# Performance work log

Measured on AMD Instinct MI355X. Metric: run time of the kernel, lower is better.

## Reference

```python
import jax, jax.numpy as jnp
import numpy as np

B, C, N, E, F = 8, 4, 2048, 512, 2048
EPS = 1e-5
MASK_SCALE = 5.0


def layer_norm(x, gamma, beta):
    mu = jnp.mean(x, axis=-1, keepdims=True)
    var = jnp.mean(jnp.square(x - mu), axis=-1, keepdims=True)
    return (x - mu) * jax.lax.rsqrt(var + EPS) * gamma + beta


def setup_inputs() -> dict:
    key = jax.random.key(0)
    ks = jax.random.split(key, 8)
    src = jax.random.normal(ks[0], (B, C, N, E), dtype=jnp.float32)
    key_padding_mask = jax.random.uniform(ks[1], (B, N), dtype=jnp.float32)
    # FFN params (torch Linear default init scale ~ U(-1/sqrt(fan_in), +))
    W1 = jax.random.normal(ks[2], (E, F), dtype=jnp.float32) / np.sqrt(E)
    b1 = jnp.zeros((F,), dtype=jnp.float32)
    W2 = jax.random.normal(ks[3], (F, E), dtype=jnp.float32) / np.sqrt(F)
    b2 = jnp.zeros((E,), dtype=jnp.float32)
    g1 = jnp.ones((E,), dtype=jnp.float32)
    be1 = jnp.zeros((E,), dtype=jnp.float32)
    g2 = jnp.ones((E,), dtype=jnp.float32)
    be2 = jnp.zeros((E,), dtype=jnp.float32)
    return {"src": src, "key_padding_mask": key_padding_mask,
            "W1": W1, "b1": b1, "W2": W2, "b2": b2,
            "g1": g1, "be1": be1, "g2": g2, "be2": be2}


def reference(src, key_padding_mask, W1, b1, W2, b2, g1, be1, g2, be2):
    # src: [B, C, N, E]; channels batched into one fused attention call
    scale = 1.0 / jnp.sqrt(jnp.asarray(src.shape[-1], src.dtype))
    scores = jnp.einsum('bcne,bcme->bcnm', src, src) * scale  # [B,C,N,N]
    scores = scores - key_padding_mask[:, None, None, :] * MASK_SCALE
    attn = jax.nn.softmax(scores, axis=-1)
    attn_out = jnp.einsum('bcnm,bcme->bcne', attn, src)
    # residual + norm1 (dropout is identity at eval)
    src2 = layer_norm(src + attn_out, g1, be1)
    # feedforward: Linear -> ReLU -> Linear
    ff = jax.nn.relu(jnp.einsum('bcne,ef->bcnf', src2, W1) + b1)
    ff = jnp.einsum('bcnf,fe->bcne', ff, W2) + b2
    out = layer_norm(src2 + ff, g2, be2)
    return out
```

## Files before the change

### kernel.cpp

```cpp
#include <hip/hip_runtime.h>
#include <stdint.h>

constexpr int CB = 8, CC = 4, CN = 2048, CE = 512, CF = 2048;
constexpr long long TOT = (long long)CB * CC * CN * CE;
constexpr int MCH = 32768;
constexpr float SCALE = 0.04419417382415922f;
constexpr float MASK_SCALE = 5.0f;
constexpr float EPS = 1e-5f;

typedef unsigned short bf16_t;
typedef __attribute__((ext_vector_type(4))) float f32x4;
typedef __attribute__((ext_vector_type(8))) short s16x8;

#define DEV static __device__ __forceinline__

DEV unsigned short f2bf(float f) {
    unsigned u = __float_as_uint(f);
    unsigned r = (u + 0x7fffu + ((u >> 16) & 1u)) >> 16;
    return (unsigned short)r;
}
DEV float bf2f(unsigned short b) {
    return __uint_as_float(((unsigned)b) << 16);
}

typedef const __attribute__((address_space(1))) unsigned int* gptr_t;
typedef __attribute__((address_space(3))) unsigned int* lptr_t;
DEV void async16(const void* g, void* l) {
    __builtin_amdgcn_global_load_lds((gptr_t)g, (lptr_t)l, 16, 0, 0);
}

#define FULL_BAR() do { asm volatile("" ::: "memory"); __builtin_amdgcn_s_barrier(); asm volatile("" ::: "memory"); } while (0)
#define LGKM0() asm volatile("s_waitcnt lgkmcnt(0)" ::: "memory")

DEV float blockSum256(float v, float* sm) {
    #pragma unroll
    for (int o = 32; o; o >>= 1) v += __shfl_xor(v, o);
    int w = threadIdx.x >> 6;
    __syncthreads();
    if ((threadIdx.x & 63) == 0) sm[w] = v;
    __syncthreads();
    return sm[0] + sm[1] + sm[2] + sm[3];
}
DEV float blockMax256(float v, float* sm) {
    #pragma unroll
    for (int o = 32; o; o >>= 1) v = fmaxf(v, __shfl_xor(v, o));
    int w = threadIdx.x >> 6;
    __syncthreads();
    if ((threadIdx.x & 63) == 0) sm[w] = v;
    __syncthreads();
    return fmaxf(fmaxf(sm[0], sm[1]), fmaxf(sm[2], sm[3]));
}

__global__ __launch_bounds__(256) void cvt_f32_bf16_vec(
    const float* __restrict__ in, bf16_t* __restrict__ out, long long n) {
    long long i = ((long long)blockIdx.x * 256 + threadIdx.x) * 4;
    long long stride = (long long)gridDim.x * 1024;
    for (; i < n; i += stride) {
        float4 v = *reinterpret_cast<const float4*>(in + i);
        ushort4 u;
        u.x = f2bf(v.x); u.y = f2bf(v.y); u.z = f2bf(v.z); u.w = f2bf(v.w);
        *reinterpret_cast<ushort4*>(out + i) = u;
    }
}

__global__ __launch_bounds__(256) void transpose_f32_bf16(
    const float* __restrict__ in, bf16_t* __restrict__ out,
    int R, int Cc) {
    __shared__ float tile[32][33];
    int rb = blockIdx.y * 32, cb = blockIdx.x * 32;
    int tx = threadIdx.x & 31, ty = threadIdx.x >> 5;
    #pragma unroll
    for (int i = 0; i < 32; i += 8)
        tile[ty + i][tx] = in[(size_t)(rb + ty + i) * Cc + cb + tx];
    __syncthreads();
    #pragma unroll
    for (int i = 0; i < 32; i += 8)
        out[(size_t)(cb + ty + i) * R + rb + tx] = f2bf(tile[tx][ty + i]);
}

__global__ __launch_bounds__(256) void transpose_bf16(
    const bf16_t* __restrict__ in, bf16_t* __restrict__ out,
    int R, int Cc, long long sIn, long long sOut) {
    __shared__ bf16_t tile[32][36];
    const bf16_t* inz = in + (size_t)blockIdx.z * sIn;
    bf16_t* outz = out + (size_t)blockIdx.z * sOut;
    int rb = blockIdx.y * 32, cb = blockIdx.x * 32;
    int t = threadIdx.x;
    int r = t >> 3, c4 = (t & 7) * 4;
    *(ushort4*)&tile[r][c4] = *(const ushort4*)&inz[(size_t)(rb + r) * Cc + cb + c4];
    __syncthreads();
    int c = t >> 3, r4 = (t & 7) * 4;
    ushort4 w;
    w.x = tile[r4 + 0][c]; w.y = tile[r4 + 1][c];
    w.z = tile[r4 + 2][c]; w.w = tile[r4 + 3][c];
    *(ushort4*)&outz[(size_t)(cb + c) * R + rb + r4] = w;
}

template <int EPI>
__global__ __launch_bounds__(512, 2) void gemm256(
    const bf16_t* __restrict__ A, const bf16_t* __restrict__ B,
    void* __restrict__ Cptr, const float* __restrict__ bias, float alpha,
    int M, int Nc, int K, long long sA, long long sB, long long sC) {
    extern __shared__ bf16_t lds[];
    bf16_t* AsL = lds;
    bf16_t* BsL = lds + 32768;

    int bx, by, bz;
    {
        int gx = gridDim.x, gy = gridDim.y;
        int nwg = gx * gy * gridDim.z;
        int flat = blockIdx.x + gx * (blockIdx.y + gy * blockIdx.z);
        int wg = (nwg & 7) ? flat : ((flat & 7) * (nwg >> 3) + (flat >> 3));
        bx = wg % gx;
        int tmp = wg / gx;
        by = tmp % gy;
        bz = tmp / gy;
    }

    const bf16_t* Az = A + (size_t)bz * sA;
    const bf16_t* Bz = B + (size_t)bz * sB;
    const int t = threadIdx.x;
    const int lane = t & 63, wid = t >> 6;
    const int wr = wid >> 2, wc = wid & 3;
    const int brow = by * 256, bcol = bx * 256;
    const int NT = K >> 6;

    const int r0 = t >> 3, s0 = t & 7;
    const int ce = ((s0 ^ (r0 & 7)) << 3);
    const bf16_t* aP0 = Az + (size_t)(brow + r0) * K + ce;
    const bf16_t* bP0 = Bz + (size_t)(bcol + r0) * K + ce;
    const size_t rK64 = (size_t)64 * K;
    const size_t h128K = (size_t)128 * K;

    #define STAGE_A(kt_, h_) do { \
        bf16_t* d_ = AsL + ((((kt_) & 1) * 2 + (h_)) * 8192); \
        const bf16_t* s_ = aP0 + (size_t)(h_) * h128K + (size_t)(kt_) * 64; \
        async16(s_, d_ + t * 8); \
        async16(s_ + rK64, d_ + 4096 + t * 8); \
    } while (0)
    #define STAGE_B(kt_, h_) do { \
        bf16_t* d_ = BsL + ((((kt_) & 1) * 2 + (h_)) * 8192); \
        const bf16_t* s_ = bP0 + (size_t)(h_) * h128K + (size_t)(kt_) * 64; \
        async16(s_, d_ + t * 8); \
        async16(s_ + rK64, d_ + 4096 + t * 8); \
    } while (0)

    const int q = lane >> 4, rr0 = lane & 15, xmask = rr0 & 7;
    s16x8 af[4][2];
    s16x8 bv[2][2][2];
    f32x4 acc[2][2][4][2] = {};

    #define READ_A(ktp_, qm_) do { \
        const bf16_t* base_ = AsL + (((ktp_) * 2 + (qm_)) * 8192); \
        _Pragma("unroll") for (int m_ = 0; m_ < 4; ++m_) \
        _Pragma("unroll") for (int ks_ = 0; ks_ < 2; ++ks_) \
            af[m_][ks_] = *(const s16x8*)(base_ + (wr * 64 + m_ * 16 + rr0) * 64 + (((ks_ * 4 + q) ^ xmask) << 3)); \
    } while (0)
    #define READ_B(ktp_, qn_) do { \
        const bf16_t* base_ = BsL + (((ktp_) * 2 + (qn_)) * 8192); \
        _Pragma("unroll") for (int n_ = 0; n_ < 2; ++n_) \
        _Pragma("unroll") for (int ks_ = 0; ks_ < 2; ++ks_) \
            bv[qn_][n_][ks_] = *(const s16x8*)(base_ + (wc * 32 + n_ * 16 + rr0) * 64 + (((ks_ * 4 + q) ^ xmask) << 3)); \
    } while (0)
    #define MFMA_Q(qm_, qn_) do { \
        __builtin_amdgcn_s_setprio(1); \
        _Pragma("unroll") for (int m_ = 0; m_ < 4; ++m_) \
        _Pragma("unroll") for (int n_ = 0; n_ < 2; ++n_) \
        _Pragma("unroll") for (int ks_ = 0; ks_ < 2; ++ks_) \
            acc[qm_][qn_][m_][n_] = __builtin_amdgcn_mfma_f32_16x16x32_bf16( \
                af[m_][ks_], bv[qn_][n_][ks_], acc[qm_][qn_][m_][n_], 0, 0, 0); \
        __builtin_amdgcn_s_setprio(0); \
    } while (0)

    STAGE_A(0, 0); STAGE_B(0, 0); STAGE_B(0, 1); STAGE_A(0, 1);
    if (1 < NT) {
        STAGE_A(1, 0); STAGE_B(1, 0);
        asm volatile("s_waitcnt vmcnt(4)" ::: "memory");
    } else {
        asm volatile("s_waitcnt vmcnt(0)" ::: "memory");
    }
    FULL_BAR();

    for (int kt = 0; kt < NT; ++kt) {
        const int ktp = kt & 1;
        READ_A(ktp, 0);
        READ_B(ktp, 0);
        if (kt + 1 < NT) STAGE_B(kt + 1, 1);
        FULL_BAR();
        LGKM0();
        MFMA_Q(0, 0);
        FULL_BAR();

        READ_B(ktp, 1);
        if (kt + 1 < NT) STAGE_A(kt + 1, 1);
        FULL_BAR();
        LGKM0();
        MFMA_Q(0, 1);
        FULL_BAR();

        READ_A(ktp, 1);
        if (kt + 2 < NT) STAGE_A(kt + 2, 0);
        FULL_BAR();
        LGKM0();
        MFMA_Q(1, 0);
        FULL_BAR();

        if (kt + 2 < NT) {
            STAGE_B(kt + 2, 0);
            asm volatile("s_waitcnt vmcnt(4)" ::: "memory");
        } else {
            asm volatile("s_waitcnt vmcnt(0)" ::: "memory");
        }
        FULL_BAR();
        MFMA_Q(1, 1);
        FULL_BAR();
    }

    size_t cz = (size_t)bz * sC;
    #pragma unroll
    for (int qm = 0; qm < 2; ++qm)
    #pragma unroll
    for (int qn = 0; qn < 2; ++qn)
    #pragma unroll
    for (int m = 0; m < 4; ++m)
    #pragma unroll
    for (int n = 0; n < 2; ++n) {
        int col = bcol + qn * 128 + wc * 32 + n * 16 + (lane & 15);
        float bvv = (EPI == 1 || EPI == 2) ? bias[col] : 0.f;
        #pragma unroll
        for (int j = 0; j < 4; ++j) {
            int row = brow + qm * 128 + wr * 64 + m * 16 + q * 4 + j;
            float v = acc[qm][qn][m][n][j] + bvv;
            if constexpr (EPI == 1)
                ((bf16_t*)Cptr)[cz + (size_t)row * Nc + col] = f2bf(fmaxf(v, 0.f));
            else if constexpr (EPI == 3)
                ((bf16_t*)Cptr)[cz + (size_t)row * Nc + col] = f2bf(v * alpha);
            else
                ((float*)Cptr)[cz + (size_t)row * Nc + col] = v;
        }
    }
    #undef STAGE_A
    #undef STAGE_B
    #undef READ_A
    #undef READ_B
    #undef MFMA_Q
}

__global__ __launch_bounds__(256) void softmax_bf16(
    bf16_t* __restrict__ S, const float* __restrict__ mask) {
    __shared__ float sm[4];
    int gr = blockIdx.x;
    int b = gr >> 13;
    bf16_t* row = S + (size_t)gr * CN;
    int tid = threadIdx.x;
    const float* mrow = mask + (size_t)b * CN + tid * 8;
    s16x8 v = *(const s16x8*)(row + tid * 8);
    float4 m0 = *(const float4*)(mrow);
    float4 m1 = *(const float4*)(mrow + 4);
    float x[8];
    x[0] = bf2f((unsigned short)v[0]) - m0.x * MASK_SCALE;
    x[1] = bf2f((unsigned short)v[1]) - m0.y * MASK_SCALE;
    x[2] = bf2f((unsigned short)v[2]) - m0.z * MASK_SCALE;
    x[3] = bf2f((unsigned short)v[3]) - m0.w * MASK_SCALE;
    x[4] = bf2f((unsigned short)v[4]) - m1.x * MASK_SCALE;
    x[5] = bf2f((unsigned short)v[5]) - m1.y * MASK_SCALE;
    x[6] = bf2f((unsigned short)v[6]) - m1.z * MASK_SCALE;
    x[7] = bf2f((unsigned short)v[7]) - m1.w * MASK_SCALE;
    float mx = -3.4e38f;
    #pragma unroll
    for (int i = 0; i < 8; i++) mx = fmaxf(mx, x[i]);
    mx = blockMax256(mx, sm);
    float s = 0.f;
    #pragma unroll
    for (int i = 0; i < 8; i++) { x[i] = __expf(x[i] - mx); s += x[i]; }
    s = blockSum256(s, sm);
    float inv = 1.f / s;
    s16x8 u;
    #pragma unroll
    for (int i = 0; i < 8; i++) u[i] = (short)f2bf(x[i] * inv);
    *(s16x8*)(row + tid * 8) = u;
}

__global__ __launch_bounds__(256) void ln1_kernel(
    const bf16_t* __restrict__ src, const bf16_t* __restrict__ ao,
    const float* __restrict__ g, const float* __restrict__ be,
    bf16_t* __restrict__ o) {
    __shared__ float sm[4];
    size_t base = (size_t)blockIdx.x * CE;
    int e = threadIdx.x * 2;
    ushort2 s = *(const ushort2*)&src[base + e];
    ushort2 a = *(const ushort2*)&ao[base + e];
    float x0 = bf2f(s.x) + bf2f(a.x), x1 = bf2f(s.y) + bf2f(a.y);
    float mu = blockSum256(x0 + x1, sm) * (1.f / CE);
    float d0 = x0 - mu, d1 = x1 - mu;
    float var = blockSum256(d0 * d0 + d1 * d1, sm) * (1.f / CE);
    float rs = rsqrtf(var + EPS);
    ushort2 w;
    w.x = f2bf(d0 * rs * g[e] + be[e]);
    w.y = f2bf(d1 * rs * g[e + 1] + be[e + 1]);
    *(ushort2*)&o[base + e] = w;
}

__global__ __launch_bounds__(256) void ln2_kernel(
    const bf16_t* __restrict__ a, const float* __restrict__ b,
    const float* __restrict__ g, const float* __restrict__ be,
    float* __restrict__ o) {
    __shared__ float sm[4];
    size_t base = (size_t)blockIdx.x * CE;
    int e = threadIdx.x * 2;
    ushort2 aa = *(const ushort2*)&a[base + e];
    float2 bb = *(const float2*)&b[base + e];
    float x0 = bf2f(aa.x) + bb.x, x1 = bf2f(aa.y) + bb.y;
    float mu = blockSum256(x0 + x1, sm) * (1.f / CE);
    float d0 = x0 - mu, d1 = x1 - mu;
    float var = blockSum256(d0 * d0 + d1 * d1, sm) * (1.f / CE);
    float rs = rsqrtf(var + EPS);
    float2 w;
    w.x = d0 * rs * g[e] + be[e];
    w.y = d1 * rs * g[e + 1] + be[e + 1];
    *(float2*)&o[base + e] = w;
}

extern "C" void kernel_launch(void* const* d_in, const int* in_sizes, int n_in,
                              void* d_out, int out_size, void* d_ws, size_t ws_size,
                              hipStream_t stream) {
    const float* src  = (const float*)d_in[0];
    const float* mask = (const float*)d_in[1];
    const float* W1   = (const float*)d_in[2];
    const float* b1   = (const float*)d_in[3];
    const float* W2   = (const float*)d_in[4];
    const float* b2   = (const float*)d_in[5];
    const float* g1   = (const float*)d_in[6];
    const float* be1  = (const float*)d_in[7];
    const float* g2   = (const float*)d_in[8];
    const float* be2  = (const float*)d_in[9];
    float* out = (float*)d_out;
    char* ws = (char*)d_ws;

    hipFuncSetAttribute(reinterpret_cast<const void*>(&gemm256<0>), hipFuncAttributeMaxDynamicSharedMemorySize, 131072);
    hipFuncSetAttribute(reinterpret_cast<const void*>(&gemm256<1>), hipFuncAttributeMaxDynamicSharedMemorySize, 131072);
    hipFuncSetAttribute(reinterpret_cast<const void*>(&gemm256<2>), hipFuncAttributeMaxDynamicSharedMemorySize, 131072);
    hipFuncSetAttribute(reinterpret_cast<const void*>(&gemm256<3>), hipFuncAttributeMaxDynamicSharedMemorySize, 131072);

    const size_t MB = 1024 * 1024;
    bf16_t* probs  = (bf16_t*)(ws);
    bf16_t* src_bf = (bf16_t*)(ws + 256 * MB);
    bf16_t* srcT   = (bf16_t*)(ws + 320 * MB);
    bf16_t* attnO  = (bf16_t*)(ws + 384 * MB);
    bf16_t* W1T    = (bf16_t*)(ws + 448 * MB);
    bf16_t* W2T    = (bf16_t*)(ws + 450 * MB);
    bf16_t* src2   = (bf16_t*)(ws);
    float*  ff     = (float*)(ws + 64 * MB);
    bf16_t* H      = (bf16_t*)(ws + 256 * MB);
    if (ws_size < 452 * MB) return;

    cvt_f32_bf16_vec<<<4096, 256, 0, stream>>>(src, src_bf, TOT);
    transpose_f32_bf16<<<dim3(CF / 32, CE / 32, 1), 256, 0, stream>>>(W1, W1T, CE, CF);
    transpose_f32_bf16<<<dim3(CE / 32, CF / 32, 1), 256, 0, stream>>>(W2, W2T, CF, CE);
    transpose_bf16<<<dim3(CE / 32, CN / 32, 32), 256, 0, stream>>>(
        src_bf, srcT, CN, CE, (long long)CN * CE, (long long)CE * CN);

    gemm256<3><<<dim3(CN / 256, CN / 256, 32), 512, 131072, stream>>>(
        src_bf, src_bf, probs, nullptr, SCALE, CN, CN, CE,
        (long long)CN * CE, (long long)CN * CE, (long long)CN * CN);
    softmax_bf16<<<dim3(CB * CC * CN), 256, 0, stream>>>(probs, mask);
    gemm256<3><<<dim3(CE / 256, CN / 256, 32), 512, 131072, stream>>>(
        probs, srcT, attnO, nullptr, 1.0f, CN, CE, CN,
        (long long)CN * CN, (long long)CE * CN, (long long)CN * CE);
    ln1_kernel<<<dim3(CB * CC * CN), 256, 0, stream>>>(src_bf, attnO, g1, be1, src2);

    for (int c = 0; c < 2; ++c) {
        const bf16_t* A2 = src2 + (size_t)c * MCH * CE;
        gemm256<1><<<dim3(CF / 256, MCH / 256, 1), 512, 131072, stream>>>(
            A2, W1T, H, b1, 1.0f, MCH, CF, CE, 0, 0, 0);
        gemm256<2><<<dim3(CE / 256, MCH / 256, 1), 512, 131072, stream>>>(
            H, W2T, ff, b2, 1.0f, MCH, CE, CF, 0, 0, 0);
        ln2_kernel<<<dim3(MCH), 256, 0, stream>>>(
            A2, ff, g2, be2, out + (size_t)c * MCH * CE);
    }
}
```

Baseline: 904.8 us.

## Restructure GEMM pipeline with fewer barriers, merge FFN passes, bf16 FFN output

The GEMM main loop now issues the next k-tile's loads in two bursts and runs two MFMA quadrants between barriers, which cuts the number of block-wide barriers per k-step. The attention GEMMs and softmax now run in two groups of 16 batch-channels, likely to keep the working set of each launch smaller. The FFN runs as a single pass over all rows instead of two chunks. The second FFN GEMM writes bf16 instead of fp32 through a new epilogue, which halves its output traffic and the matching read in the final layer norm, at some cost in accuracy.

```diff
diff --git a/kernel.cpp b/kernel.cpp
--- a/kernel.cpp
+++ b/kernel.cpp
@@ -3,7 +3,8 @@
 
 constexpr int CB = 8, CC = 4, CN = 2048, CE = 512, CF = 2048;
 constexpr long long TOT = (long long)CB * CC * CN * CE;
-constexpr int MCH = 32768;
+constexpr int GRP = 16;
+constexpr int MCH = 65536;
 constexpr float SCALE = 0.04419417382415922f;
 constexpr float MASK_SCALE = 5.0f;
 constexpr float EPS = 1e-5f;
@@ -142,6 +143,13 @@
         bf16_t* d_ = BsL + ((((kt_) & 1) * 2 + (h_)) * 8192); \
         const bf16_t* s_ = bP0 + (size_t)(h_) * h128K + (size_t)(kt_) * 64; \
         async16(s_, d_ + t * 8); \
+        async16(s_ + 4096 + t * 8, d_ + 4096 + t * 8); \
+    } while (0)
+    #undef STAGE_B
+    #define STAGE_B(kt_, h_) do { \
+        bf16_t* d_ = BsL + ((((kt_) & 1) * 2 + (h_)) * 8192); \
+        const bf16_t* s_ = bP0 + (size_t)(h_) * h128K + (size_t)(kt_) * 64; \
+        async16(s_, d_ + t * 8); \
         async16(s_ + rK64, d_ + 4096 + t * 8); \
     } while (0)
 
@@ -173,47 +181,33 @@
     } while (0)
 
     STAGE_A(0, 0); STAGE_B(0, 0); STAGE_B(0, 1); STAGE_A(0, 1);
-    if (1 < NT) {
-        STAGE_A(1, 0); STAGE_B(1, 0);
-        asm volatile("s_waitcnt vmcnt(4)" ::: "memory");
-    } else {
-        asm volatile("s_waitcnt vmcnt(0)" ::: "memory");
-    }
+    asm volatile("s_waitcnt vmcnt(2)" ::: "memory");
     FULL_BAR();
 
     for (int kt = 0; kt < NT; ++kt) {
         const int ktp = kt & 1;
         READ_A(ktp, 0);
         READ_B(ktp, 0);
-        if (kt + 1 < NT) STAGE_B(kt + 1, 1);
-        FULL_BAR();
-        LGKM0();
-        MFMA_Q(0, 0);
-        FULL_BAR();
-
         READ_B(ktp, 1);
-        if (kt + 1 < NT) STAGE_A(kt + 1, 1);
-        FULL_BAR();
-        LGKM0();
-        MFMA_Q(0, 1);
-        FULL_BAR();
-
-        READ_A(ktp, 1);
-        if (kt + 2 < NT) STAGE_A(kt + 2, 0);
-        FULL_BAR();
-        LGKM0();
-        MFMA_Q(1, 0);
-        FULL_BAR();
-
-        if (kt + 2 < NT) {
-            STAGE_B(kt + 2, 0);
-            asm volatile("s_waitcnt vmcnt(4)" ::: "memory");
+        if (kt + 1 < NT) {
+            STAGE_A(kt + 1, 0); STAGE_B(kt + 1, 0); STAGE_B(kt + 1, 1);
+            asm volatile("s_waitcnt vmcnt(6)" ::: "memory");
         } else {
             asm volatile("s_waitcnt vmcnt(0)" ::: "memory");
         }
         FULL_BAR();
+        LGKM0();
+        MFMA_Q(0, 0);
+        MFMA_Q(0, 1);
+        READ_A(ktp, 1);
+        if (kt + 1 < NT) {
+            STAGE_A(kt + 1, 1);
+            asm volatile("s_waitcnt vmcnt(2)" ::: "memory");
+        }
+        FULL_BAR();
+        LGKM0();
+        MFMA_Q(1, 0);
         MFMA_Q(1, 1);
-        FULL_BAR();
     }
 
     size_t cz = (size_t)bz * sC;
@@ -226,7 +220,7 @@
     #pragma unroll
     for (int n = 0; n < 2; ++n) {
         int col = bcol + qn * 128 + wc * 32 + n * 16 + (lane & 15);
-        float bvv = (EPI == 1 || EPI == 2) ? bias[col] : 0.f;
+        float bvv = (EPI == 1 || EPI == 2 || EPI == 4) ? bias[col] : 0.f;
         #pragma unroll
         for (int j = 0; j < 4; ++j) {
             int row = brow + qm * 128 + wr * 64 + m * 16 + q * 4 + j;
@@ -235,6 +229,8 @@
                 ((bf16_t*)Cptr)[cz + (size_t)row * Nc + col] = f2bf(fmaxf(v, 0.f));
             else if constexpr (EPI == 3)
                 ((bf16_t*)Cptr)[cz + (size_t)row * Nc + col] = f2bf(v * alpha);
+            else if constexpr (EPI == 4)
+                ((bf16_t*)Cptr)[cz + (size_t)row * Nc + col] = f2bf(v);
             else
                 ((float*)Cptr)[cz + (size_t)row * Nc + col] = v;
         }
@@ -247,10 +243,10 @@
 }
 
 __global__ __launch_bounds__(256) void softmax_bf16(
-    bf16_t* __restrict__ S, const float* __restrict__ mask) {
+    bf16_t* __restrict__ S, const float* __restrict__ mask, int bc0) {
     __shared__ float sm[4];
     int gr = blockIdx.x;
-    int b = gr >> 13;
+    int b = (bc0 + (gr >> 11)) >> 2;
     bf16_t* row = S + (size_t)gr * CN;
     int tid = threadIdx.x;
     const float* mrow = mask + (size_t)b * CN + tid * 8;
@@ -302,15 +298,15 @@
 }
 
 __global__ __launch_bounds__(256) void ln2_kernel(
-    const bf16_t* __restrict__ a, const float* __restrict__ b,
+    const bf16_t* __restrict__ a, const bf16_t* __restrict__ b,
     const float* __restrict__ g, const float* __restrict__ be,
     float* __restrict__ o) {
     __shared__ float sm[4];
     size_t base = (size_t)blockIdx.x * CE;
     int e = threadIdx.x * 2;
     ushort2 aa = *(const ushort2*)&a[base + e];
-    float2 bb = *(const float2*)&b[base + e];
-    float x0 = bf2f(aa.x) + bb.x, x1 = bf2f(aa.y) + bb.y;
+    ushort2 bb = *(const ushort2*)&b[base + e];
+    float x0 = bf2f(aa.x) + bf2f(bb.x), x1 = bf2f(aa.y) + bf2f(bb.y);
     float mu = blockSum256(x0 + x1, sm) * (1.f / CE);
     float d0 = x0 - mu, d1 = x1 - mu;
     float var = blockSum256(d0 * d0 + d1 * d1, sm) * (1.f / CE);
@@ -337,10 +333,9 @@
     float* out = (float*)d_out;
     char* ws = (char*)d_ws;
 
-    hipFuncSetAttribute(reinterpret_cast<const void*>(&gemm256<0>), hipFuncAttributeMaxDynamicSharedMemorySize, 131072);
     hipFuncSetAttribute(reinterpret_cast<const void*>(&gemm256<1>), hipFuncAttributeMaxDynamicSharedMemorySize, 131072);
-    hipFuncSetAttribute(reinterpret_cast<const void*>(&gemm256<2>), hipFuncAttributeMaxDynamicSharedMemorySize, 131072);
     hipFuncSetAttribute(reinterpret_cast<const void*>(&gemm256<3>), hipFuncAttributeMaxDynamicSharedMemorySize, 131072);
+    hipFuncSetAttribute(reinterpret_cast<const void*>(&gemm256<4>), hipFuncAttributeMaxDynamicSharedMemorySize, 131072);
 
     const size_t MB = 1024 * 1024;
     bf16_t* probs  = (bf16_t*)(ws);
@@ -350,8 +345,8 @@
     bf16_t* W1T    = (bf16_t*)(ws + 448 * MB);
     bf16_t* W2T    = (bf16_t*)(ws + 450 * MB);
     bf16_t* src2   = (bf16_t*)(ws);
-    float*  ff     = (float*)(ws + 64 * MB);
-    bf16_t* H      = (bf16_t*)(ws + 256 * MB);
+    bf16_t* ff     = (bf16_t*)(ws + 64 * MB);
+    bf16_t* H      = (bf16_t*)(ws + 128 * MB);
     if (ws_size < 452 * MB) return;
 
     cvt_f32_bf16_vec<<<4096, 256, 0, stream>>>(src, src_bf, TOT);
@@ -360,22 +355,23 @@
     transpose_bf16<<<dim3(CE / 32, CN / 32, 32), 256, 0, stream>>>(
         src_bf, srcT, CN, CE, (long long)CN * CE, (long long)CE * CN);
 
-    gemm256<3><<<dim3(CN / 256, CN / 256, 32), 512, 131072, stream>>>(
-        src_bf, src_bf, probs, nullptr, SCALE, CN, CN, CE,
-        (long long)CN * CE, (long long)CN * CE, (long long)CN * CN);
-    softmax_bf16<<<dim3(CB * CC * CN), 256, 0, stream>>>(probs, mask);
-    gemm256<3><<<dim3(CE / 256, CN / 256, 32), 512, 131072, stream>>>(
-        probs, srcT, attnO, nullptr, 1.0f, CN, CE, CN,
-        (long long)CN * CN, (long long)CE * CN, (long long)CN * CE);
+    for (int g0 = 0; g0 < CB * CC; g0 += GRP) {
+        const bf16_t* srcb = src_bf + (size_t)g0 * CN * CE;
+        bf16_t* probs_g = probs + (size_t)g0 * CN * CN;
+        gemm256<3><<<dim3(CN / 256, CN / 256, GRP), 512, 131072, stream>>>(
+            srcb, srcb, probs_g, nullptr, SCALE, CN, CN, CE,
+            (long long)CN * CE, (long long)CN * CE, (long long)CN * CN);
+        softmax_bf16<<<dim3(GRP * CN), 256, 0, stream>>>(probs_g, mask, g0);
+        gemm256<3><<<dim3(CE / 256, CN / 256, GRP), 512, 131072, stream>>>(
+            probs_g, srcT + (size_t)g0 * CE * CN, attnO + (size_t)g0 * CN * CE,
+            nullptr, 1.0f, CN, CE, CN,
+            (long long)CN * CN, (long long)CE * CN, (long long)CN * CE);
+    }
     ln1_kernel<<<dim3(CB * CC * CN), 256, 0, stream>>>(src_bf, attnO, g1, be1, src2);
 
-    for (int c = 0; c < 2; ++c) {
-        const bf16_t* A2 = src2 + (size_t)c * MCH * CE;
-        gemm256<1><<<dim3(CF / 256, MCH / 256, 1), 512, 131072, stream>>>(
-            A2, W1T, H, b1, 1.0f, MCH, CF, CE, 0, 0, 0);
-        gemm256<2><<<dim3(CE / 256, MCH / 256, 1), 512, 131072, stream>>>(
-            H, W2T, ff, b2, 1.0f, MCH, CE, CF, 0, 0, 0);
-        ln2_kernel<<<dim3(MCH), 256, 0, stream>>>(
-            A2, ff, g2, be2, out + (size_t)c * MCH * CE);
-    }
-}
+    gemm256<1><<<dim3(CF / 256, MCH / 256, 1), 512, 131072, stream>>>(
+        src2, W1T, H, b1, 1.0f, MCH, CF, CE, 0, 0, 0);
+    gemm256<4><<<dim3(CE / 256, MCH / 256, 1), 512, 131072, stream>>>(
+        H, W2T, ff, b2, 1.0f, MCH, CE, CF, 0, 0, 0);
+    ln2_kernel<<<dim3(MCH), 256, 0, stream>>>(src2, ff, g2, be2, out);
+}
```

Result: no change. 891.5 us (-1.5%).
